# Kernel tuning notes

Hardware: AMD Instinct MI355X
Metric: run time of the kernel (lower is better)

Reference implementation:

```python
import jax, jax.numpy as jnp
import numpy as np

B, T, N, IN_DIM, HID = 32, 24, 512, 64, 128


def setup_inputs() -> dict:
    key = jax.random.key(0)
    ks = jax.random.split(key, 7)
    s_in = 1.0 / np.sqrt(IN_DIM)
    s_h = 1.0 / np.sqrt(HID)
    x = jax.random.normal(ks[0], (B, T, N, IN_DIM), jnp.float32)
    W_mlp = jax.random.uniform(ks[1], (HID, IN_DIM), jnp.float32, -s_in, s_in)
    b_mlp = jax.random.uniform(ks[2], (HID,), jnp.float32, -s_in, s_in)
    W_ih = jax.random.uniform(ks[3], (3 * HID, HID), jnp.float32, -s_h, s_h)
    W_hh = jax.random.uniform(ks[4], (3 * HID, HID), jnp.float32, -s_h, s_h)
    b_ih = jax.random.uniform(ks[5], (3 * HID,), jnp.float32, -s_h, s_h)
    b_hh = jax.random.uniform(ks[6], (3 * HID,), jnp.float32, -s_h, s_h)
    return {"x": x, "W_mlp": W_mlp, "b_mlp": b_mlp,
            "W_ih": W_ih, "W_hh": W_hh, "b_ih": b_ih, "b_hh": b_hh}


def reference(x, W_mlp, b_mlp, W_ih, W_hh, b_ih, b_hh):
    # x: [B, T, N, IN] -> Linear + ReLU -> [B, T, N, H]
    Bv, Tv, Nv, _ = x.shape
    H = W_mlp.shape[0]
    embs = jax.nn.relu(jnp.einsum('btnf,hf->btnh', x, W_mlp) + b_mlp)
    # time-major sequence of flattened (B*N) batch, matching h_in = x[:, t].reshape(-1, in_dim)
    seq = embs.transpose(1, 0, 2, 3).reshape(Tv, Bv * Nv, H)

    def gru_step(h, xt):
        gi = xt @ W_ih.T + b_ih        # [BN, 3H]
        gh = h @ W_hh.T + b_hh         # [BN, 3H]
        i_r, i_z, i_n = jnp.split(gi, 3, axis=-1)
        h_r, h_z, h_n = jnp.split(gh, 3, axis=-1)
        r = jax.nn.sigmoid(i_r + h_r)
        z = jax.nn.sigmoid(i_z + h_z)
        n = jnp.tanh(i_n + r * h_n)
        h_new = (1.0 - z) * n + z * h  # PyTorch GRUCell update
        return h_new, None

    h0 = jnp.zeros((Bv * Nv, H), dtype=x.dtype)
    h_final, _ = jax.lax.scan(gru_step, h0, seq)
    return h_final.reshape(Bv, Nv, H)
```

## Files before the change

### kernel.cpp

```cpp
#include <hip/hip_runtime.h>
#include <hip/hip_bf16.h>

#define T_STEPS 24
#define NB      512
#define HID     128
#define INDIM   64
#define BN      16384

typedef __bf16 bf16_t;
typedef __bf16 bf16x8 __attribute__((ext_vector_type(8)));
typedef float  f32x16 __attribute__((ext_vector_type(16)));

__device__ __forceinline__ float rcp_(float x) { return __builtin_amdgcn_rcpf(x); }
__device__ __forceinline__ float sigm_(float x) { return rcp_(1.f + __expf(-x)); }
__device__ __forceinline__ float tanh_(float x) { return fmaf(2.f, rcp_(1.f + __expf(-2.f * x)), -1.f); }

#define MF(a, b, c) __builtin_amdgcn_mfma_f32_32x32x16_bf16((a), (b), (c), 0, 0, 0)

#define BARRIER_LDS() do { \
    asm volatile("s_waitcnt lgkmcnt(0)" ::: "memory"); \
    __builtin_amdgcn_s_barrier(); \
    __builtin_amdgcn_sched_barrier(0); \
} while (0)

__global__ void pack_kernel(const float* __restrict__ Wm,
                            const float* __restrict__ Wih, const float* __restrict__ Whh,
                            const float* __restrict__ bih, const float* __restrict__ bhh,
                            bf16_t* __restrict__ Wrz, bf16_t* __restrict__ Win,
                            bf16_t* __restrict__ Whn, bf16_t* __restrict__ WmP,
                            float* __restrict__ bc)
{
    int tid = blockIdx.x * 256 + threadIdx.x;
    if (tid < 65536) {
        int e = tid & 7, l = (tid >> 3) & 63, ks = (tid >> 9) & 15, ct = tid >> 13;
        int col = ct * 32 + (l & 31);
        int k   = ks * 16 + ((l >> 5) << 3) + e;
        float v = (k < 128) ? Wih[col * HID + k] : Whh[col * HID + (k - 128)];
        Wrz[tid] = (bf16_t)v;
    } else if (tid < 81920) {
        int u = tid - 65536;
        int e = u & 7, l = (u >> 3) & 63, ks = (u >> 9) & 7, ct = u >> 12;
        int col = ct * 32 + (l & 31);
        int k   = ks * 16 + ((l >> 5) << 3) + e;
        Win[u] = (bf16_t)Wih[(256 + col) * HID + k];
    } else if (tid < 98304) {
        int u = tid - 81920;
        int e = u & 7, l = (u >> 3) & 63, ks = (u >> 9) & 7, ct = u >> 12;
        int col = ct * 32 + (l & 31);
        int k   = ks * 16 + ((l >> 5) << 3) + e;
        Whn[u] = (bf16_t)Whh[(256 + col) * HID + k];
    } else if (tid < 106496) {
        int u = tid - 98304;
        int e = u & 7, l = (u >> 3) & 63, ks = (u >> 9) & 3, ct = u >> 11;
        int col = ct * 32 + (l & 31);
        int k   = ks * 16 + ((l >> 5) << 3) + e;
        WmP[u] = (bf16_t)Wm[col * INDIM + k];
    } else if (tid < 107008) {
        int j = tid - 106496;
        float v;
        if (j < 256)      v = bih[j] + bhh[j];
        else if (j < 384) v = bih[j];
        else              v = bhh[j - 128];
        bc[j] = v;
    }
}

__global__ __launch_bounds__(512)
__attribute__((amdgpu_waves_per_eu(2, 2)))
void gru_all(
    const float*  __restrict__ x, float* __restrict__ out,
    const bf16_t* __restrict__ Wrz, const bf16_t* __restrict__ Win,
    const bf16_t* __restrict__ Whn, const bf16_t* __restrict__ WmP,
    const float*  __restrict__ bc,  const float* __restrict__ bm)
{
    __shared__ __align__(16) char WinS[32768];
    __shared__ __align__(16) char WhnS[32768];
    __shared__ __align__(16) char es0[16384], es1[16384];
    __shared__ __align__(16) char hs0[16384], hs1[16384];
    __shared__ __align__(16) char xs0[8192],  xs1[8192];

    const int tid = threadIdx.x;
    const int l   = tid & 63;
    const int w   = tid >> 6;
    const int rt  = w >> 2;
    const int ct  = w & 3;
    const int r0  = blockIdx.x * 64;
    const int b   = r0 >> 9;
    const int n0  = r0 & (NB - 1);

    const int lane31 = l & 31;
    const int hi     = l >> 5;
    const int rA     = rt * 32 + lane31;
    const int sw0    = (lane31 & 15) << 4;
    const int jh     = ct * 32 + lane31;

    const int xrow  = w * 8 + (l >> 3);
    const int xslot = l & 7;
    const int xsWr  = xrow * 128 + (((xslot ^ (xrow & 7))) << 4);
    const char* xb0 = (const char*)(x + ((size_t)b * T_STEPS * NB + n0) * INDIM);
    const int  xgOff = xrow * 256 + xslot * 32;
    const size_t xstep = (size_t)NB * INDIM * 4;

    {
        const uint4* s; uint4* d;
        s = (const uint4*)Win; d = (uint4*)WinS;
        for (int i = tid; i < 2048; i += 512) d[i] = s[i];
        s = (const uint4*)Whn; d = (uint4*)WhnS;
        for (int i = tid; i < 2048; i += 512) d[i] = s[i];
        uint4 z4 = make_uint4(0, 0, 0, 0);
        for (int i = tid; i < 1024; i += 512) ((uint4*)hs0)[i] = z4;
    }
    bf16x8 wmp0 = *(const bf16x8*)(WmP + (ct * 4 + 0) * 512 + l * 8);
    bf16x8 wmp1 = *(const bf16x8*)(WmP + (ct * 4 + 1) * 512 + l * 8);
    bf16x8 wmp2 = *(const bf16x8*)(WmP + (ct * 4 + 2) * 512 + l * 8);
    bf16x8 wmp3 = *(const bf16x8*)(WmP + (ct * 4 + 3) * 512 + l * 8);

    const float bRr = bc[jh], bRz = bc[128 + jh];
    const float bIN = bc[256 + jh], bHN = bc[384 + jh];
    const float bmv = bm[jh];

    const bf16_t* wrR = Wrz + (ct * 16) * 512 + l * 8;
    const bf16_t* wrZ = Wrz + ((ct + 4) * 16) * 512 + l * 8;
    #define LDG(p) (*(const bf16x8*)(p))

    #define XLOAD(T_, A_, B_) { \
        const char* xp = xb0 + (size_t)(T_) * xstep + xgOff; \
        A_ = *(const float4*)(xp); B_ = *(const float4*)(xp + 16); }
    #define XWRITE(DST, A_, B_) { \
        union { bf16_t h8[8]; uint4 u; } pk; \
        pk.h8[0] = (bf16_t)(A_).x; pk.h8[1] = (bf16_t)(A_).y; \
        pk.h8[2] = (bf16_t)(A_).z; pk.h8[3] = (bf16_t)(A_).w; \
        pk.h8[4] = (bf16_t)(B_).x; pk.h8[5] = (bf16_t)(B_).y; \
        pk.h8[6] = (bf16_t)(B_).z; pk.h8[7] = (bf16_t)(B_).w; \
        *(uint4*)((DST) + xsWr) = pk.u; }

    #define PHASE_A(XSRC, EDST) { \
        f32x16 accA; \
        _Pragma("unroll") for (int q = 0; q < 16; ++q) accA[q] = bmv; \
        { bf16x8 a0 = *(const bf16x8*)((XSRC) + rA * 128 + ((((0*2+hi) ^ (rA & 7))) << 4)); \
          accA = MF(a0, wmp0, accA); \
          bf16x8 a1 = *(const bf16x8*)((XSRC) + rA * 128 + ((((1*2+hi) ^ (rA & 7))) << 4)); \
          accA = MF(a1, wmp1, accA); \
          bf16x8 a2 = *(const bf16x8*)((XSRC) + rA * 128 + ((((2*2+hi) ^ (rA & 7))) << 4)); \
          accA = MF(a2, wmp2, accA); \
          bf16x8 a3 = *(const bf16x8*)((XSRC) + rA * 128 + ((((3*2+hi) ^ (rA & 7))) << 4)); \
          accA = MF(a3, wmp3, accA); } \
        _Pragma("unroll") for (int q = 0; q < 16; ++q) { \
            int rl  = (q & 3) + ((q >> 2) << 3) + (hi << 2); \
            int row = rt * 32 + rl; \
            *(bf16_t*)((EDST) + row * 256 + ((jh * 2) ^ ((rl & 15) << 4))) = \
                (bf16_t)fmaxf(accA[q], 0.f); } }

    f32x16 h = {};

    {
        float4 pa, pb;
        XLOAD(0, pa, pb);
        XWRITE(xs0, pa, pb);
        float4 pc, pd;
        XLOAD(1, pc, pd);
        BARRIER_LDS();
        PHASE_A(xs0, es0);
        XWRITE(xs1, pc, pd);
    }

    #pragma unroll 1
    for (int t = 0; t < T_STEPS; ++t) {
        const char* esC = (t & 1) ? es1 : es0;
        char*       esN = (t & 1) ? es0 : es1;
        const char* hsC = (t & 1) ? hs1 : hs0;
        char*       hsN = (t & 1) ? hs0 : hs1;
        char*       xsW = (t & 1) ? xs1 : xs0;
        const char* xsA = (t & 1) ? xs0 : xs1;

        BARRIER_LDS();

        f32x16 ar, az, ai, ah;
        #pragma unroll
        for (int q = 0; q < 16; ++q) { ar[q] = bRr; az[q] = bRz; ai[q] = bIN; ah[q] = bHN; }
        #pragma unroll 2
        for (int kk = 0; kk < 8; ++kk) {
            int off = ((kk * 2 + hi) * 16) ^ sw0;
            bf16x8 aE  = *(const bf16x8*)(esC + rA * 256 + off);
            bf16x8 aH  = *(const bf16x8*)(hsC + rA * 256 + off);
            bf16x8 bRe = LDG(wrR + kk * 512);
            bf16x8 bRh = LDG(wrR + (8 + kk) * 512);
            bf16x8 bZe = LDG(wrZ + kk * 512);
            bf16x8 bZh = LDG(wrZ + (8 + kk) * 512);
            bf16x8 bI  = *(const bf16x8*)(WinS + (ct * 8 + kk) * 1024 + l * 16);
            bf16x8 bN  = *(const bf16x8*)(WhnS + (ct * 8 + kk) * 1024 + l * 16);
            ar = MF(aE, bRe, ar); ar = MF(aH, bRh, ar);
            az = MF(aE, bZe, az); az = MF(aH, bZh, az);
            ai = MF(aE, bI,  ai); ah = MF(aH, bN,  ah);
        }

        float4 pxA, pxB;
        const bool havex = (t + 2 < T_STEPS);
        if (havex) XLOAD(t + 2, pxA, pxB);

        if (t + 1 < T_STEPS) PHASE_A(xsA, esN);

        #pragma unroll
        for (int q = 0; q < 16; ++q) {
            int rl  = (q & 3) + ((q >> 2) << 3) + (hi << 2);
            int row = rt * 32 + rl;
            float r  = sigm_(ar[q]);
            float z  = sigm_(az[q]);
            float n  = tanh_(ai[q] + r * ah[q]);
            float hv = n + z * (h[q] - n);
            h[q] = hv;
            *(bf16_t*)(hsN + row * 256 + ((jh * 2) ^ ((rl & 15) << 4))) = (bf16_t)hv;
        }

        if (havex) XWRITE(xsW, pxA, pxB);
    }

    #pragma unroll
    for (int q = 0; q < 16; ++q) {
        int rl = (q & 3) + ((q >> 2) << 3) + (hi << 2);
        out[(size_t)(r0 + rt * 32 + rl) * HID + jh] = h[q];
    }
    #undef LDG
    #undef XLOAD
    #undef XWRITE
    #undef PHASE_A
}

extern "C" void kernel_launch(void* const* d_in, const int* in_sizes, int n_in,
                              void* d_out, int out_size, void* d_ws, size_t ws_size,
                              hipStream_t stream)
{
    const float* x   = (const float*)d_in[0];
    const float* Wm  = (const float*)d_in[1];
    const float* bm  = (const float*)d_in[2];
    const float* Wih = (const float*)d_in[3];
    const float* Whh = (const float*)d_in[4];
    const float* bih = (const float*)d_in[5];
    const float* bhh = (const float*)d_in[6];

    char* ws = (char*)d_ws;
    bf16_t* Wrz = (bf16_t*)(ws);
    bf16_t* Win = (bf16_t*)(ws + 131072);
    bf16_t* Whn = (bf16_t*)(ws + 163840);
    bf16_t* WmP = (bf16_t*)(ws + 196608);
    float*  bcp = (float*) (ws + 212992);

    pack_kernel<<<418, 256, 0, stream>>>(Wm, Wih, Whh, bih, bhh, Wrz, Win, Whn, WmP, bcp);
    gru_all<<<256, 512, 0, stream>>>(x, (float*)d_out, Wrz, Win, Whn, WmP, bcp, bm);
}
```

Baseline: 123.7 us.

## Switch GRU kernel to 16x16x32 MFMA with 16 waves per block

Replaces the 32x32x16 MFMA tiling with 16x16x32 MFMA tiles. Each block now runs 1024 threads (16 waves), each owning 32 rows by 16 hidden columns, and all packed weight layouts are regenerated to match. The aim is more waves per block to hide latency during the sequential time loop and to cut the per-wave register footprint. In exchange, each wave issues more MFMA instructions and more LDS A-fragment loads, and only half the threads take part in the x prefetch.

New measurement: 287.1 us. +132.1%, slower.

```diff
diff --git a/kernel.cpp b/kernel.cpp
--- a/kernel.cpp
+++ b/kernel.cpp
@@ -9,13 +9,13 @@
 
 typedef __bf16 bf16_t;
 typedef __bf16 bf16x8 __attribute__((ext_vector_type(8)));
-typedef float  f32x16 __attribute__((ext_vector_type(16)));
+typedef float  f32x4  __attribute__((ext_vector_type(4)));
 
 __device__ __forceinline__ float rcp_(float x) { return __builtin_amdgcn_rcpf(x); }
 __device__ __forceinline__ float sigm_(float x) { return rcp_(1.f + __expf(-x)); }
 __device__ __forceinline__ float tanh_(float x) { return fmaf(2.f, rcp_(1.f + __expf(-2.f * x)), -1.f); }
 
-#define MF(a, b, c) __builtin_amdgcn_mfma_f32_32x32x16_bf16((a), (b), (c), 0, 0, 0)
+#define MF16(a, b, c) __builtin_amdgcn_mfma_f32_16x16x32_bf16((a), (b), (c), 0, 0, 0)
 
 #define BARRIER_LDS() do { \
     asm volatile("s_waitcnt lgkmcnt(0)" ::: "memory"); \
@@ -32,28 +32,28 @@
 {
     int tid = blockIdx.x * 256 + threadIdx.x;
     if (tid < 65536) {
-        int e = tid & 7, l = (tid >> 3) & 63, ks = (tid >> 9) & 15, ct = tid >> 13;
-        int col = ct * 32 + (l & 31);
-        int k   = ks * 16 + ((l >> 5) << 3) + e;
+        int e = tid & 7, l = (tid >> 3) & 63, ks = (tid >> 9) & 7, g = tid >> 12;
+        int col = (g & 7) * 16 + (l & 15) + ((g >> 3) << 7);
+        int k   = ks * 32 + ((l >> 4) << 3) + e;
         float v = (k < 128) ? Wih[col * HID + k] : Whh[col * HID + (k - 128)];
         Wrz[tid] = (bf16_t)v;
     } else if (tid < 81920) {
         int u = tid - 65536;
-        int e = u & 7, l = (u >> 3) & 63, ks = (u >> 9) & 7, ct = u >> 12;
-        int col = ct * 32 + (l & 31);
-        int k   = ks * 16 + ((l >> 5) << 3) + e;
+        int e = u & 7, l = (u >> 3) & 63, ks = (u >> 9) & 3, ct = u >> 11;
+        int col = ct * 16 + (l & 15);
+        int k   = ks * 32 + ((l >> 4) << 3) + e;
         Win[u] = (bf16_t)Wih[(256 + col) * HID + k];
     } else if (tid < 98304) {
         int u = tid - 81920;
-        int e = u & 7, l = (u >> 3) & 63, ks = (u >> 9) & 7, ct = u >> 12;
-        int col = ct * 32 + (l & 31);
-        int k   = ks * 16 + ((l >> 5) << 3) + e;
+        int e = u & 7, l = (u >> 3) & 63, ks = (u >> 9) & 3, ct = u >> 11;
+        int col = ct * 16 + (l & 15);
+        int k   = ks * 32 + ((l >> 4) << 3) + e;
         Whn[u] = (bf16_t)Whh[(256 + col) * HID + k];
     } else if (tid < 106496) {
         int u = tid - 98304;
-        int e = u & 7, l = (u >> 3) & 63, ks = (u >> 9) & 3, ct = u >> 11;
-        int col = ct * 32 + (l & 31);
-        int k   = ks * 16 + ((l >> 5) << 3) + e;
+        int e = u & 7, l = (u >> 3) & 63, ks = (u >> 9) & 1, ct = u >> 10;
+        int col = ct * 16 + (l & 15);
+        int k   = ks * 32 + ((l >> 4) << 3) + e;
         WmP[u] = (bf16_t)Wm[col * INDIM + k];
     } else if (tid < 107008) {
         int j = tid - 106496;
@@ -65,8 +65,8 @@
     }
 }
 
-__global__ __launch_bounds__(512)
-__attribute__((amdgpu_waves_per_eu(2, 2)))
+__global__ __launch_bounds__(1024)
+__attribute__((amdgpu_waves_per_eu(4, 4)))
 void gru_all(
     const float*  __restrict__ x, float* __restrict__ out,
     const bf16_t* __restrict__ Wrz, const bf16_t* __restrict__ Win,
@@ -82,21 +82,22 @@
     const int tid = threadIdx.x;
     const int l   = tid & 63;
     const int w   = tid >> 6;
-    const int rt  = w >> 2;
-    const int ct  = w & 3;
+    const int rt  = w >> 3;
+    const int ct  = w & 7;
     const int r0  = blockIdx.x * 64;
     const int b   = r0 >> 9;
     const int n0  = r0 & (NB - 1);
 
-    const int lane31 = l & 31;
-    const int hi     = l >> 5;
-    const int rA     = rt * 32 + lane31;
-    const int sw0    = (lane31 & 15) << 4;
-    const int jh     = ct * 32 + lane31;
-
-    const int xrow  = w * 8 + (l >> 3);
-    const int xslot = l & 7;
-    const int xsWr  = xrow * 128 + (((xslot ^ (xrow & 7))) << 4);
+    const int l16 = l & 15;
+    const int lj  = l >> 4;
+    const int row0 = rt * 32 + l16;
+    const int row1 = row0 + 16;
+    const int sw   = l16 << 4;
+    const int jh   = ct * 16 + l16;
+
+    const int xrow  = tid >> 3;
+    const int xslot = tid & 7;
+    const int xsWr  = xrow * 128 + ((xslot ^ (xrow & 7)) << 4);
     const char* xb0 = (const char*)(x + ((size_t)b * T_STEPS * NB + n0) * INDIM);
     const int  xgOff = xrow * 256 + xslot * 32;
     const size_t xstep = (size_t)NB * INDIM * 4;
@@ -104,23 +105,20 @@
     {
         const uint4* s; uint4* d;
         s = (const uint4*)Win; d = (uint4*)WinS;
-        for (int i = tid; i < 2048; i += 512) d[i] = s[i];
+        for (int i = tid; i < 2048; i += 1024) d[i] = s[i];
         s = (const uint4*)Whn; d = (uint4*)WhnS;
-        for (int i = tid; i < 2048; i += 512) d[i] = s[i];
-        uint4 z4 = make_uint4(0, 0, 0, 0);
-        for (int i = tid; i < 1024; i += 512) ((uint4*)hs0)[i] = z4;
-    }
-    bf16x8 wmp0 = *(const bf16x8*)(WmP + (ct * 4 + 0) * 512 + l * 8);
-    bf16x8 wmp1 = *(const bf16x8*)(WmP + (ct * 4 + 1) * 512 + l * 8);
-    bf16x8 wmp2 = *(const bf16x8*)(WmP + (ct * 4 + 2) * 512 + l * 8);
-    bf16x8 wmp3 = *(const bf16x8*)(WmP + (ct * 4 + 3) * 512 + l * 8);
+        for (int i = tid; i < 2048; i += 1024) d[i] = s[i];
+        ((uint4*)hs0)[tid] = make_uint4(0, 0, 0, 0);
+    }
+    bf16x8 wmp0 = *(const bf16x8*)(WmP + (ct * 2 + 0) * 512 + l * 8);
+    bf16x8 wmp1 = *(const bf16x8*)(WmP + (ct * 2 + 1) * 512 + l * 8);
 
     const float bRr = bc[jh], bRz = bc[128 + jh];
     const float bIN = bc[256 + jh], bHN = bc[384 + jh];
     const float bmv = bm[jh];
 
-    const bf16_t* wrR = Wrz + (ct * 16) * 512 + l * 8;
-    const bf16_t* wrZ = Wrz + ((ct + 4) * 16) * 512 + l * 8;
+    const bf16_t* wrR = Wrz + (ct * 8) * 512 + l * 8;
+    const bf16_t* wrZ = Wrz + ((8 + ct) * 8) * 512 + l * 8;
     #define LDG(p) (*(const bf16x8*)(p))
 
     #define XLOAD(T_, A_, B_) { \
@@ -135,33 +133,27 @@
         *(uint4*)((DST) + xsWr) = pk.u; }
 
     #define PHASE_A(XSRC, EDST) { \
-        f32x16 accA; \
-        _Pragma("unroll") for (int q = 0; q < 16; ++q) accA[q] = bmv; \
-        { bf16x8 a0 = *(const bf16x8*)((XSRC) + rA * 128 + ((((0*2+hi) ^ (rA & 7))) << 4)); \
-          accA = MF(a0, wmp0, accA); \
-          bf16x8 a1 = *(const bf16x8*)((XSRC) + rA * 128 + ((((1*2+hi) ^ (rA & 7))) << 4)); \
-          accA = MF(a1, wmp1, accA); \
-          bf16x8 a2 = *(const bf16x8*)((XSRC) + rA * 128 + ((((2*2+hi) ^ (rA & 7))) << 4)); \
-          accA = MF(a2, wmp2, accA); \
-          bf16x8 a3 = *(const bf16x8*)((XSRC) + rA * 128 + ((((3*2+hi) ^ (rA & 7))) << 4)); \
-          accA = MF(a3, wmp3, accA); } \
-        _Pragma("unroll") for (int q = 0; q < 16; ++q) { \
-            int rl  = (q & 3) + ((q >> 2) << 3) + (hi << 2); \
-            int row = rt * 32 + rl; \
-            *(bf16_t*)((EDST) + row * 256 + ((jh * 2) ^ ((rl & 15) << 4))) = \
-                (bf16_t)fmaxf(accA[q], 0.f); } }
-
-    f32x16 h = {};
+        f32x4 aA0 = {bmv, bmv, bmv, bmv}, aA1 = aA0; \
+        { bf16x8 a00 = *(const bf16x8*)((XSRC) + row0 * 128 + (((0 + lj) ^ (row0 & 7)) << 4)); \
+          bf16x8 a10 = *(const bf16x8*)((XSRC) + row1 * 128 + (((0 + lj) ^ (row1 & 7)) << 4)); \
+          aA0 = MF16(a00, wmp0, aA0); aA1 = MF16(a10, wmp0, aA1); \
+          bf16x8 a01 = *(const bf16x8*)((XSRC) + row0 * 128 + (((4 + lj) ^ (row0 & 7)) << 4)); \
+          bf16x8 a11 = *(const bf16x8*)((XSRC) + row1 * 128 + (((4 + lj) ^ (row1 & 7)) << 4)); \
+          aA0 = MF16(a01, wmp1, aA0); aA1 = MF16(a11, wmp1, aA1); } \
+        _Pragma("unroll") for (int rg = 0; rg < 4; ++rg) { \
+            int rl = lj * 4 + rg; \
+            int sb = (jh * 2) ^ (rl << 4); \
+            *(bf16_t*)((EDST) + (rt * 32 + rl) * 256 + sb)      = (bf16_t)fmaxf(aA0[rg], 0.f); \
+            *(bf16_t*)((EDST) + (rt * 32 + 16 + rl) * 256 + sb) = (bf16_t)fmaxf(aA1[rg], 0.f); } }
+
+    f32x4 h0 = {}, h1 = {};
 
     {
-        float4 pa, pb;
-        XLOAD(0, pa, pb);
-        XWRITE(xs0, pa, pb);
-        float4 pc, pd;
-        XLOAD(1, pc, pd);
+        float4 pa, pb, pc, pd;
+        if (tid < 512) { XLOAD(0, pa, pb); XWRITE(xs0, pa, pb); XLOAD(1, pc, pd); }
         BARRIER_LDS();
         PHASE_A(xs0, es0);
-        XWRITE(xs1, pc, pd);
+        if (tid < 512) XWRITE(xs1, pc, pd);
     }
 
     #pragma unroll 1
@@ -175,50 +167,67 @@
 
         BARRIER_LDS();
 
-        f32x16 ar, az, ai, ah;
+        f32x4 ar0 = {bRr, bRr, bRr, bRr}, ar1 = ar0;
+        f32x4 az0 = {bRz, bRz, bRz, bRz}, az1 = az0;
+        f32x4 ai0 = {bIN, bIN, bIN, bIN}, ai1 = ai0;
+        f32x4 ah0 = {bHN, bHN, bHN, bHN}, ah1 = ah0;
         #pragma unroll
-        for (int q = 0; q < 16; ++q) { ar[q] = bRr; az[q] = bRz; ai[q] = bIN; ah[q] = bHN; }
-        #pragma unroll 2
-        for (int kk = 0; kk < 8; ++kk) {
-            int off = ((kk * 2 + hi) * 16) ^ sw0;
-            bf16x8 aE  = *(const bf16x8*)(esC + rA * 256 + off);
-            bf16x8 aH  = *(const bf16x8*)(hsC + rA * 256 + off);
-            bf16x8 bRe = LDG(wrR + kk * 512);
-            bf16x8 bRh = LDG(wrR + (8 + kk) * 512);
-            bf16x8 bZe = LDG(wrZ + kk * 512);
-            bf16x8 bZh = LDG(wrZ + (8 + kk) * 512);
-            bf16x8 bI  = *(const bf16x8*)(WinS + (ct * 8 + kk) * 1024 + l * 16);
-            bf16x8 bN  = *(const bf16x8*)(WhnS + (ct * 8 + kk) * 1024 + l * 16);
-            ar = MF(aE, bRe, ar); ar = MF(aH, bRh, ar);
-            az = MF(aE, bZe, az); az = MF(aH, bZh, az);
-            ai = MF(aE, bI,  ai); ah = MF(aH, bN,  ah);
+        for (int kk = 0; kk < 4; ++kk) {
+            int off = (kk * 64 + lj * 16) ^ sw;
+            bf16x8 aE0 = *(const bf16x8*)(esC + row0 * 256 + off);
+            bf16x8 aE1 = *(const bf16x8*)(esC + row1 * 256 + off);
+            bf16x8 wr  = LDG(wrR + kk * 512);
+            bf16x8 wz  = LDG(wrZ + kk * 512);
+            bf16x8 wi  = *(const bf16x8*)(WinS + (ct * 4 + kk) * 1024 + l * 16);
+            ar0 = MF16(aE0, wr, ar0); ar1 = MF16(aE1, wr, ar1);
+            az0 = MF16(aE0, wz, az0); az1 = MF16(aE1, wz, az1);
+            ai0 = MF16(aE0, wi, ai0); ai1 = MF16(aE1, wi, ai1);
         }
+        #pragma unroll
+        for (int kk = 0; kk < 4; ++kk) {
+            int off = (kk * 64 + lj * 16) ^ sw;
+            bf16x8 aH0 = *(const bf16x8*)(hsC + row0 * 256 + off);
+            bf16x8 aH1 = *(const bf16x8*)(hsC + row1 * 256 + off);
+            bf16x8 wr  = LDG(wrR + (4 + kk) * 512);
+            bf16x8 wz  = LDG(wrZ + (4 + kk) * 512);
+            bf16x8 wn  = *(const bf16x8*)(WhnS + (ct * 4 + kk) * 1024 + l * 16);
+            ar0 = MF16(aH0, wr, ar0); ar1 = MF16(aH1, wr, ar1);
+            az0 = MF16(aH0, wz, az0); az1 = MF16(aH1, wz, az1);
+            ah0 = MF16(aH0, wn, ah0); ah1 = MF16(aH1, wn, ah1);
+        }
 
         float4 pxA, pxB;
-        const bool havex = (t + 2 < T_STEPS);
+        const bool havex = (t + 2 < T_STEPS) && (tid < 512);
         if (havex) XLOAD(t + 2, pxA, pxB);
 
         if (t + 1 < T_STEPS) PHASE_A(xsA, esN);
 
         #pragma unroll
-        for (int q = 0; q < 16; ++q) {
-            int rl  = (q & 3) + ((q >> 2) << 3) + (hi << 2);
-            int row = rt * 32 + rl;
-            float r  = sigm_(ar[q]);
-            float z  = sigm_(az[q]);
-            float n  = tanh_(ai[q] + r * ah[q]);
-            float hv = n + z * (h[q] - n);
-            h[q] = hv;
-            *(bf16_t*)(hsN + row * 256 + ((jh * 2) ^ ((rl & 15) << 4))) = (bf16_t)hv;
+        for (int rg = 0; rg < 4; ++rg) {
+            int rl = lj * 4 + rg;
+            int sb = (jh * 2) ^ (rl << 4);
+            float r  = sigm_(ar0[rg]);
+            float z  = sigm_(az0[rg]);
+            float n  = tanh_(ai0[rg] + r * ah0[rg]);
+            float hv = n + z * (h0[rg] - n);
+            h0[rg] = hv;
+            *(bf16_t*)(hsN + (rt * 32 + rl) * 256 + sb) = (bf16_t)hv;
+            float r1 = sigm_(ar1[rg]);
+            float z1 = sigm_(az1[rg]);
+            float n1 = tanh_(ai1[rg] + r1 * ah1[rg]);
+            float hv1 = n1 + z1 * (h1[rg] - n1);
+            h1[rg] = hv1;
+            *(bf16_t*)(hsN + (rt * 32 + 16 + rl) * 256 + sb) = (bf16_t)hv1;
         }
 
         if (havex) XWRITE(xsW, pxA, pxB);
     }
 
     #pragma unroll
-    for (int q = 0; q < 16; ++q) {
-        int rl = (q & 3) + ((q >> 2) << 3) + (hi << 2);
-        out[(size_t)(r0 + rt * 32 + rl) * HID + jh] = h[q];
+    for (int rg = 0; rg < 4; ++rg) {
+        int rl = lj * 4 + rg;
+        out[(size_t)(r0 + rt * 32 + rl) * HID + jh]      = h0[rg];
+        out[(size_t)(r0 + rt * 32 + 16 + rl) * HID + jh] = h1[rg];
     }
     #undef LDG
     #undef XLOAD
@@ -246,5 +255,5 @@
     float*  bcp = (float*) (ws + 212992);
 
     pack_kernel<<<418, 256, 0, stream>>>(Wm, Wih, Whh, bih, bhh, Wrz, Win, Whn, WmP, bcp);
-    gru_all<<<256, 512, 0, stream>>>(x, (float*)d_out, Wrz, Win, Whn, WmP, bcp, bm);
+    gru_all<<<256, 1024, 0, stream>>>(x, (float*)d_out, Wrz, Win, Whn, WmP, bcp, bm);
 }
```
